# Kernel tuning notes

Measured on AMD Instinct MI355X. Metric: run time of the kernel, lower is better.

## Reference

```python
import jax, jax.numpy as jnp
import numpy as np

R = 16
LORA_ALPHA = 16
SCALING = LORA_ALPHA / R  # 1.0


def setup_inputs() -> dict:
    key = jax.random.key(0)
    kx, kr, ka = jax.random.split(key, 3)
    B, S, D, DO, E = 4, 2048, 4096, 4096, 8
    x = jax.random.normal(kx, (B, S, D), dtype=jnp.float32)
    # kaiming_uniform_(a=sqrt(5)) on Linear weight of fan_in=D -> U(-1/sqrt(D), 1/sqrt(D))
    bound_r = 1.0 / np.sqrt(D)
    route_w = jax.random.uniform(kr, (E, D), jnp.float32, -bound_r, bound_r)  # lora_route.weight
    bound_a = 1.0 / np.sqrt(D)
    A = jax.random.uniform(ka, (E, R, D), jnp.float32, -bound_a, bound_a)  # stacked lora_A{i}.weight [r, D]
    # lora_B weights are zero-initialized in the module; use small random for a nontrivial baseline
    kb = jax.random.fold_in(key, 7)
    Bw = jax.random.normal(kb, (E, DO, R), dtype=jnp.float32) * 0.02  # stacked lora_B{i}.weight [DO, r]
    return {"x": x, "route_w": route_w, "A": A, "Bw": Bw}


def reference(x, route_w, A, Bw):
    # router logits [B, S, E]
    logits = jnp.einsum("bsd,ed->bse", x, route_w)
    # top-1 hard routing: keep raw logit value at the argmax slot, zero elsewhere
    topk_v, topk_idx = jax.lax.top_k(logits, 1)  # [B,S,1]
    E = logits.shape[-1]
    route_weight = jax.nn.one_hot(topk_idx[..., 0], E, dtype=logits.dtype) * topk_v  # [B,S,E]
    # low-rank per-expert projections (dense over experts, as in the original loop)
    h = jnp.einsum("bsd,erd->bser", x, A)            # [B,S,E,r]
    wh = route_weight[..., None] * h                  # weight before the up-projection
    out = jnp.einsum("bser,eor->bso", wh, Bw) * SCALING  # [B,S,DO]
    return out
```

## Files before the change

### kernel.cpp

```cpp
#include <hip/hip_runtime.h>
#include <hip/hip_bf16.h>

#define DD   4096
#define NE   8
#define NR   16
#define NTOK 8192
#define NDO  4096
#define TAU  0.01f
#define MAXFLAG 8000

typedef __attribute__((ext_vector_type(8))) __bf16 bf16x8;
typedef __attribute__((ext_vector_type(4))) __bf16 bf16x4;
typedef __attribute__((ext_vector_type(4))) float  f32x4;

__device__ __forceinline__ bf16x8 to_bf16x8(float4 a, float4 b) {
    bf16x8 r;
    r[0] = (__bf16)a.x; r[1] = (__bf16)a.y; r[2] = (__bf16)a.z; r[3] = (__bf16)a.w;
    r[4] = (__bf16)b.x; r[5] = (__bf16)b.y; r[6] = (__bf16)b.z; r[7] = (__bf16)b.w;
    return r;
}

__device__ __forceinline__ bf16x8 zero_frag() {
    bf16x8 z;
    #pragma unroll
    for (int j = 0; j < 8; j++) z[j] = (__bf16)0.0f;
    return z;
}

__global__ __launch_bounds__(256) void k_prep_w(const float* __restrict__ rw,
                                                const float* __restrict__ Am,
                                                const float* __restrict__ Bw,
                                                __bf16* __restrict__ rwhl,
                                                __bf16* __restrict__ Ab,
                                                __bf16* __restrict__ Bwb) {
    const int b = blockIdx.x;
    if (b < 1024) {
        const int o = (b & 511) * 1024 + threadIdx.x * 4;
        const float4 v = *(const float4*)(((b < 512) ? Bw : Am) + o);
        bf16x4 p;
        p[0] = (__bf16)v.x; p[1] = (__bf16)v.y; p[2] = (__bf16)v.z; p[3] = (__bf16)v.w;
        *(bf16x4*)(((b < 512) ? Bwb : Ab) + o) = p;
    } else {
        const int o = (b - 1024) * 1024 + threadIdx.x * 4;
        const int row = o >> 12, k = o & 4095;
        const float4 v = *(const float4*)(rw + ((size_t)(row & 7) << 12) + k);
        bf16x4 p;
        if (row < 8) {
            p[0] = (__bf16)v.x; p[1] = (__bf16)v.y; p[2] = (__bf16)v.z; p[3] = (__bf16)v.w;
        } else {
            p[0] = (__bf16)(v.x - (float)(__bf16)v.x);
            p[1] = (__bf16)(v.y - (float)(__bf16)v.y);
            p[2] = (__bf16)(v.z - (float)(__bf16)v.z);
            p[3] = (__bf16)(v.w - (float)(__bf16)v.w);
        }
        *(bf16x4*)(rwhl + o) = p;
    }
}

__global__ __launch_bounds__(256, 1) void k_route(const float* __restrict__ x,
                                                  const __bf16* __restrict__ rwhl,
                                                  float* __restrict__ w_arr,
                                                  int*   __restrict__ token_list,
                                                  int*   __restrict__ count,
                                                  int*   __restrict__ nflag,
                                                  int*   __restrict__ flaglist) {
    const int t0   = blockIdx.x * 16;
    const int wv   = threadIdx.x >> 6;
    const int lane = threadIdx.x & 63;
    const int m    = lane & 15;
    const int half = lane >> 4;

    const float*  xrow = x    + (size_t)(t0 + m) * DD;
    const __bf16* wrow = rwhl + (size_t)m * DD;

    f32x4 acc = {0.f, 0.f, 0.f, 0.f};
    const int kbase = wv * 1024;
    for (int g = 0; g < 8; g++) {
        float4 xa[4], xc[4]; bf16x8 wb[4];
        #pragma unroll
        for (int i = 0; i < 4; i++) {
            const int k0 = kbase + (g * 4 + i) * 32 + half * 8;
            xa[i] = *(const float4*)(xrow + k0);
            xc[i] = *(const float4*)(xrow + k0 + 4);
            wb[i] = *(const bf16x8*)(wrow + k0);
        }
        #pragma unroll
        for (int i = 0; i < 4; i++)
            acc = __builtin_amdgcn_mfma_f32_16x16x32_bf16(to_bf16x8(xa[i], xc[i]), wb[i], acc, 0, 0, 0);
    }

    __shared__ float Lred[4][16][17];
    #pragma unroll
    for (int r = 0; r < 4; r++)
        Lred[wv][half * 4 + r][m] = acc[r];
    __syncthreads();

    __shared__ float logitS[16][NE];
    if (threadIdx.x < 128) {
        const int t = threadIdx.x >> 3, ee = threadIdx.x & 7;
        float s = 0.f;
        #pragma unroll
        for (int w = 0; w < 4; w++) s += Lred[w][t][ee] + Lred[w][t][ee + 8];
        logitS[t][ee] = s;
    }
    __syncthreads();

    if (threadIdx.x < 16) {
        const int t = threadIdx.x;
        float best = -1e30f, second = -1e30f; int be = 0;
        #pragma unroll
        for (int e = 0; e < NE; e++) {
            const float s = logitS[t][e];
            if (s > best) { second = best; best = s; be = e; }
            else if (s > second) { second = s; }
        }
        const int tok = t0 + t;
        w_arr[tok] = best;
        if (best - second < TAU) {
            const int p = atomicAdd(nflag, 1);
            if (p < MAXFLAG) flaglist[p] = tok;
        } else {
            const int p = atomicAdd(&count[be], 1);
            token_list[be * NTOK + p] = tok;
        }
    }
}

__global__ __launch_bounds__(256) void k_fix(const float* __restrict__ x,
                                             const float* __restrict__ rw,
                                             float* __restrict__ w_arr,
                                             int*   __restrict__ token_list,
                                             int*   __restrict__ count,
                                             const int* __restrict__ nflag,
                                             const int* __restrict__ flaglist) {
    const int wv   = threadIdx.x >> 6;
    const int lane = threadIdx.x & 63;
    int n = *nflag; if (n > MAXFLAG) n = MAXFLAG;

    for (int idx = blockIdx.x * 4 + wv; idx < n; idx += 512) {
        const int tok = flaglist[idx];
        const float* xp = x + (size_t)tok * DD;
        double acc[NE];
        #pragma unroll
        for (int e = 0; e < NE; e++) acc[e] = 0.0;
        for (int i = 0; i < 16; i++) {
            const int d4 = (i * 64 + lane) * 4;
            const float4 xv = *(const float4*)(xp + d4);
            const double x0 = xv.x, x1 = xv.y, x2 = xv.z, x3 = xv.w;
            #pragma unroll
            for (int e = 0; e < NE; e++) {
                const float4 wv4 = *(const float4*)(rw + (size_t)e * DD + d4);
                acc[e] = fma(x0, (double)wv4.x, acc[e]);
                acc[e] = fma(x1, (double)wv4.y, acc[e]);
                acc[e] = fma(x2, (double)wv4.z, acc[e]);
                acc[e] = fma(x3, (double)wv4.w, acc[e]);
            }
        }
        #pragma unroll
        for (int off = 32; off > 0; off >>= 1)
            #pragma unroll
            for (int e = 0; e < NE; e++)
                acc[e] += __shfl_xor(acc[e], off, 64);
        if (lane == 0) {
            double best = acc[0]; int be = 0;
            #pragma unroll
            for (int e = 1; e < NE; e++) if (acc[e] > best) { best = acc[e]; be = e; }
            w_arr[tok] = (float)best;
            const int pos = atomicAdd(&count[be], 1);
            token_list[be * NTOK + pos] = tok;
        }
    }
}

__global__ __launch_bounds__(1024) void k_h(const float* __restrict__ x,
                                            const __bf16* __restrict__ Ab,
                                            const float* __restrict__ w_arr,
                                            const int*   __restrict__ token_list,
                                            const int*   __restrict__ count,
                                            __hip_bfloat16* __restrict__ wh) {
    const int e    = blockIdx.x >> 7;
    const int g    = blockIdx.x & 127;
    const int cnt  = count[e];
    const int base = g * 32;
    if (base >= cnt) return;

    const int wv   = threadIdx.x >> 6;
    const int lane = threadIdx.x & 63;
    const int m    = lane & 15;
    const int half = lane >> 4;

    const int i0 = base + m,  i1 = base + 16 + m;
    const int tok0 = (i0 < cnt) ? token_list[e * NTOK + i0] : 0;
    const int tok1 = (i1 < cnt) ? token_list[e * NTOK + i1] : 0;
    const float*  xr0  = x  + (size_t)tok0 * DD;
    const float*  xr1  = x  + (size_t)tok1 * DD;
    const __bf16* arow = Ab + ((size_t)e * NR + m) * DD;

    f32x4 acc0 = {0.f,0.f,0.f,0.f}, acc1 = {0.f,0.f,0.f,0.f};
    const int kbase = wv * 256;
    #pragma unroll
    for (int kc = 0; kc < 8; kc++) {
        const int k0 = kbase + kc * 32 + half * 8;
        const bf16x8 bfrag = *(const bf16x8*)(arow + k0);
        const bf16x8 a0 = to_bf16x8(*(const float4*)(xr0 + k0),
                                    *(const float4*)(xr0 + k0 + 4));
        const bf16x8 a1 = to_bf16x8(*(const float4*)(xr1 + k0),
                                    *(const float4*)(xr1 + k0 + 4));
        acc0 = __builtin_amdgcn_mfma_f32_16x16x32_bf16(a0, bfrag, acc0, 0, 0, 0);
        acc1 = __builtin_amdgcn_mfma_f32_16x16x32_bf16(a1, bfrag, acc1, 0, 0, 0);
    }

    __shared__ float lds[16][32][17];
    #pragma unroll
    for (int rr = 0; rr < 4; rr++) {
        lds[wv][half * 4 + rr][m]      = acc0[rr];
        lds[wv][16 + half * 4 + rr][m] = acc1[rr];
    }
    __syncthreads();

    if (threadIdx.x < 512) {
        const int t = threadIdx.x >> 4;
        const int r = threadIdx.x & 15;
        const int i2 = base + t;
        if (i2 < cnt) {
            float s = 0.f;
            #pragma unroll
            for (int w = 0; w < 16; w++) s += lds[w][t][r];
            const int tk = token_list[e * NTOK + i2];
            wh[(size_t)tk * NR + r] = (__hip_bfloat16)(s * w_arr[tk]);
        }
    }
}

__global__ __launch_bounds__(256, 1) void k_out(const __bf16* __restrict__ Bwb,
                                                const __hip_bfloat16* __restrict__ wh,
                                                const int*   __restrict__ token_list,
                                                const int*   __restrict__ count,
                                                float* __restrict__ out) {
    const int bx    = blockIdx.x;
    const int chunk = bx & 3;
    const int slot  = (bx >> 2) & 511;
    const int e     = bx >> 11;
    const int cnt   = count[e];
    const int base  = slot * 16;
    if (base >= cnt) return;

    const int wv   = threadIdx.x >> 6;
    const int lane = threadIdx.x & 63;
    const int m    = lane & 15;
    const int half = lane >> 4;

    const int  idx   = base + m;
    const bool valid = idx < cnt;
    const int  tok   = valid ? token_list[e * NTOK + idx] : 0;
    const bf16x8 zf  = zero_frag();

    const bf16x8 a2 = (half < 2 && valid)
        ? *(const bf16x8*)((const __bf16*)wh + (size_t)tok * NR + half * 8)
        : zf;

    int trow[4]; bool vrow[4];
    #pragma unroll
    for (int r = 0; r < 4; r++) {
        const int ir = base + half * 4 + r;
        vrow[r] = ir < cnt;
        trow[r] = vrow[r] ? token_list[e * NTOK + ir] : 0;
    }

    const __bf16* bwe = Bwb + (size_t)e * NDO * NR;
    const int h2 = (half < 2) ? half : 0;
    const f32x4 zero4 = {0.f, 0.f, 0.f, 0.f};
    const int ob0 = chunk * 1024 + wv * 256;

    for (int g = 0; g < 2; g++) {
        bf16x8 B[8];
        #pragma unroll
        for (int i = 0; i < 8; i++) {
            const int obase = ob0 + (g * 8 + i) * 16;
            B[i] = (half < 2)
                ? *(const bf16x8*)(bwe + (size_t)(obase + m) * NR + h2 * 8)
                : zf;
        }
        #pragma unroll
        for (int i = 0; i < 8; i++) {
            const int obase = ob0 + (g * 8 + i) * 16;
            const f32x4 d = __builtin_amdgcn_mfma_f32_16x16x32_bf16(a2, B[i], zero4, 0, 0, 0);
            #pragma unroll
            for (int r = 0; r < 4; r++) {
                if (vrow[r])
                    __builtin_nontemporal_store(d[r], &out[(size_t)trow[r] * NDO + obase + m]);
            }
        }
    }
}

extern "C" void kernel_launch(void* const* d_in, const int* in_sizes, int n_in,
                              void* d_out, int out_size, void* d_ws, size_t ws_size,
                              hipStream_t stream) {
    const float* x  = (const float*)d_in[0];
    const float* rw = (const float*)d_in[1];
    const float* Am = (const float*)d_in[2];
    const float* Bw = (const float*)d_in[3];
    float* out = (float*)d_out;

    char* ws = (char*)d_ws;
    int*   count      = (int*)ws;
    int*   nflag      = (int*)(ws + 32);
    float* w_arr      = (float*)(ws + 512);
    int*   flaglist   = (int*)(ws + 33280);
    int*   token_list = (int*)(ws + 65536);
    __hip_bfloat16* wh = (__hip_bfloat16*)(ws + 327680);
    __bf16* rwhl      = (__bf16*)(ws + 589824);
    __bf16* Bwb       = (__bf16*)(ws + 720896);
    __bf16* Ab        = (__bf16*)(ws + 1769472);

    hipMemsetAsync(ws, 0, 64, stream);
    hipLaunchKernelGGL(k_prep_w, dim3(1088),  dim3(256),  0, stream, rw, Am, Bw, rwhl, Ab, Bwb);
    hipLaunchKernelGGL(k_route,  dim3(512),   dim3(256),  0, stream, x, rwhl, w_arr, token_list, count, nflag, flaglist);
    hipLaunchKernelGGL(k_fix,    dim3(128),   dim3(256),  0, stream, x, rw, w_arr, token_list, count, nflag, flaglist);
    hipLaunchKernelGGL(k_h,      dim3(1024),  dim3(1024), 0, stream, x, Ab, w_arr, token_list, count, wh);
    hipLaunchKernelGGL(k_out,    dim3(16384), dim3(256),  0, stream, Bwb, wh, token_list, count, out);
}
```

Baseline: 161.1 us.

## Split router GEMV over K across blocks and stage k_out stores through LDS

The router logit computation is split into four K-slices per token group, giving 2048 blocks instead of 512. Partial logits go to a workspace buffer, and a small finalize kernel sums them and does the top-1 selection and token bucketing. Separately, k_out now writes its MFMA results into a shared-memory tile and then emits full contiguous 1024-wide rows per token, replacing scattered per-lane stores. This adds a kernel launch, a partial-sum round trip through global memory, and about 64KB of LDS per k_out block, which may limit occupancy.

```diff
diff --git a/kernel.cpp b/kernel.cpp
--- a/kernel.cpp
+++ b/kernel.cpp
@@ -57,36 +57,29 @@
     }
 }
 
-__global__ __launch_bounds__(256, 1) void k_route(const float* __restrict__ x,
-                                                  const __bf16* __restrict__ rwhl,
-                                                  float* __restrict__ w_arr,
-                                                  int*   __restrict__ token_list,
-                                                  int*   __restrict__ count,
-                                                  int*   __restrict__ nflag,
-                                                  int*   __restrict__ flaglist) {
-    const int t0   = blockIdx.x * 16;
-    const int wv   = threadIdx.x >> 6;
+__global__ __launch_bounds__(256, 1) void k_route_part(const float* __restrict__ x,
+                                                       const __bf16* __restrict__ rwhl,
+                                                       float* __restrict__ pbuf) {
+    const int tg = blockIdx.x >> 2;
+    const int kg = blockIdx.x & 3;
+    const int t0 = tg * 16;
+    const int wv = threadIdx.x >> 6;
     const int lane = threadIdx.x & 63;
-    const int m    = lane & 15;
+    const int m = lane & 15;
     const int half = lane >> 4;
 
     const float*  xrow = x    + (size_t)(t0 + m) * DD;
     const __bf16* wrow = rwhl + (size_t)m * DD;
 
     f32x4 acc = {0.f, 0.f, 0.f, 0.f};
-    const int kbase = wv * 1024;
-    for (int g = 0; g < 8; g++) {
-        float4 xa[4], xc[4]; bf16x8 wb[4];
-        #pragma unroll
-        for (int i = 0; i < 4; i++) {
-            const int k0 = kbase + (g * 4 + i) * 32 + half * 8;
-            xa[i] = *(const float4*)(xrow + k0);
-            xc[i] = *(const float4*)(xrow + k0 + 4);
-            wb[i] = *(const bf16x8*)(wrow + k0);
-        }
-        #pragma unroll
-        for (int i = 0; i < 4; i++)
-            acc = __builtin_amdgcn_mfma_f32_16x16x32_bf16(to_bf16x8(xa[i], xc[i]), wb[i], acc, 0, 0, 0);
+    const int kbase = kg * 1024 + wv * 256;
+    #pragma unroll
+    for (int ks = 0; ks < 8; ks++) {
+        const int k0 = kbase + ks * 32 + half * 8;
+        const float4 xa = *(const float4*)(xrow + k0);
+        const float4 xc = *(const float4*)(xrow + k0 + 4);
+        const bf16x8 wb = *(const bf16x8*)(wrow + k0);
+        acc = __builtin_amdgcn_mfma_f32_16x16x32_bf16(to_bf16x8(xa, xc), wb, acc, 0, 0, 0);
     }
 
     __shared__ float Lred[4][16][17];
@@ -95,34 +88,43 @@
         Lred[wv][half * 4 + r][m] = acc[r];
     __syncthreads();
 
-    __shared__ float logitS[16][NE];
     if (threadIdx.x < 128) {
         const int t = threadIdx.x >> 3, ee = threadIdx.x & 7;
         float s = 0.f;
         #pragma unroll
         for (int w = 0; w < 4; w++) s += Lred[w][t][ee] + Lred[w][t][ee + 8];
-        logitS[t][ee] = s;
-    }
-    __syncthreads();
-
-    if (threadIdx.x < 16) {
-        const int t = threadIdx.x;
-        float best = -1e30f, second = -1e30f; int be = 0;
-        #pragma unroll
-        for (int e = 0; e < NE; e++) {
-            const float s = logitS[t][e];
-            if (s > best) { second = best; best = s; be = e; }
-            else if (s > second) { second = s; }
-        }
-        const int tok = t0 + t;
-        w_arr[tok] = best;
-        if (best - second < TAU) {
-            const int p = atomicAdd(nflag, 1);
-            if (p < MAXFLAG) flaglist[p] = tok;
-        } else {
-            const int p = atomicAdd(&count[be], 1);
-            token_list[be * NTOK + p] = tok;
-        }
+        pbuf[((size_t)kg * NTOK + t0 + t) * NE + ee] = s;
+    }
+}
+
+__global__ __launch_bounds__(256) void k_route_fin(const float* __restrict__ pbuf,
+                                                   float* __restrict__ w_arr,
+                                                   int*   __restrict__ token_list,
+                                                   int*   __restrict__ count,
+                                                   int*   __restrict__ nflag,
+                                                   int*   __restrict__ flaglist) {
+    const int tok = blockIdx.x * 256 + threadIdx.x;
+    float l[NE];
+    #pragma unroll
+    for (int e = 0; e < NE; e++)
+        l[e] = pbuf[((size_t)0 * NTOK + tok) * NE + e]
+             + pbuf[((size_t)1 * NTOK + tok) * NE + e]
+             + pbuf[((size_t)2 * NTOK + tok) * NE + e]
+             + pbuf[((size_t)3 * NTOK + tok) * NE + e];
+
+    float best = -1e30f, second = -1e30f; int be = 0;
+    #pragma unroll
+    for (int e = 0; e < NE; e++) {
+        if (l[e] > best) { second = best; best = l[e]; be = e; }
+        else if (l[e] > second) { second = l[e]; }
+    }
+    w_arr[tok] = best;
+    if (best - second < TAU) {
+        const int p = atomicAdd(nflag, 1);
+        if (p < MAXFLAG) flaglist[p] = tok;
+    } else {
+        const int p = atomicAdd(&count[be], 1);
+        token_list[be * NTOK + p] = tok;
     }
 }
 
@@ -259,37 +261,43 @@
         ? *(const bf16x8*)((const __bf16*)wh + (size_t)tok * NR + half * 8)
         : zf;
 
-    int trow[4]; bool vrow[4];
-    #pragma unroll
-    for (int r = 0; r < 4; r++) {
-        const int ir = base + half * 4 + r;
-        vrow[r] = ir < cnt;
-        trow[r] = vrow[r] ? token_list[e * NTOK + ir] : 0;
-    }
-
+    __shared__ float lds[16][1028];
     const __bf16* bwe = Bwb + (size_t)e * NDO * NR;
     const int h2 = (half < 2) ? half : 0;
     const f32x4 zero4 = {0.f, 0.f, 0.f, 0.f};
-    const int ob0 = chunk * 1024 + wv * 256;
+    const int ob0 = wv * 256;
 
     for (int g = 0; g < 2; g++) {
         bf16x8 B[8];
         #pragma unroll
         for (int i = 0; i < 8; i++) {
-            const int obase = ob0 + (g * 8 + i) * 16;
+            const int oc = chunk * 1024 + ob0 + (g * 8 + i) * 16;
             B[i] = (half < 2)
-                ? *(const bf16x8*)(bwe + (size_t)(obase + m) * NR + h2 * 8)
+                ? *(const bf16x8*)(bwe + (size_t)(oc + m) * NR + h2 * 8)
                 : zf;
         }
         #pragma unroll
         for (int i = 0; i < 8; i++) {
-            const int obase = ob0 + (g * 8 + i) * 16;
             const f32x4 d = __builtin_amdgcn_mfma_f32_16x16x32_bf16(a2, B[i], zero4, 0, 0, 0);
-            #pragma unroll
-            for (int r = 0; r < 4; r++) {
-                if (vrow[r])
-                    __builtin_nontemporal_store(d[r], &out[(size_t)trow[r] * NDO + obase + m]);
-            }
+            const int col = ob0 + (g * 8 + i) * 16 + m;
+            #pragma unroll
+            for (int r = 0; r < 4; r++)
+                lds[half * 4 + r][col] = d[r];
+        }
+    }
+    __syncthreads();
+
+    #pragma unroll 4
+    for (int r = 0; r < 16; r++) {
+        const int ir = base + r;
+        if (ir < cnt) {
+            const int tr = token_list[e * NTOK + ir];
+            const float4 v = *(const float4*)&lds[r][threadIdx.x * 4];
+            float* dst = out + (size_t)tr * NDO + chunk * 1024 + threadIdx.x * 4;
+            __builtin_nontemporal_store(v.x, dst + 0);
+            __builtin_nontemporal_store(v.y, dst + 1);
+            __builtin_nontemporal_store(v.z, dst + 2);
+            __builtin_nontemporal_store(v.w, dst + 3);
         }
     }
 }
@@ -313,11 +321,13 @@
     __bf16* rwhl      = (__bf16*)(ws + 589824);
     __bf16* Bwb       = (__bf16*)(ws + 720896);
     __bf16* Ab        = (__bf16*)(ws + 1769472);
+    float*  pbuf      = (float*)(ws + 3145728);
 
     hipMemsetAsync(ws, 0, 64, stream);
-    hipLaunchKernelGGL(k_prep_w, dim3(1088),  dim3(256),  0, stream, rw, Am, Bw, rwhl, Ab, Bwb);
-    hipLaunchKernelGGL(k_route,  dim3(512),   dim3(256),  0, stream, x, rwhl, w_arr, token_list, count, nflag, flaglist);
-    hipLaunchKernelGGL(k_fix,    dim3(128),   dim3(256),  0, stream, x, rw, w_arr, token_list, count, nflag, flaglist);
-    hipLaunchKernelGGL(k_h,      dim3(1024),  dim3(1024), 0, stream, x, Ab, w_arr, token_list, count, wh);
-    hipLaunchKernelGGL(k_out,    dim3(16384), dim3(256),  0, stream, Bwb, wh, token_list, count, out);
-}
+    hipLaunchKernelGGL(k_prep_w,     dim3(1088),  dim3(256), 0, stream, rw, Am, Bw, rwhl, Ab, Bwb);
+    hipLaunchKernelGGL(k_route_part, dim3(2048),  dim3(256), 0, stream, x, rwhl, pbuf);
+    hipLaunchKernelGGL(k_route_fin,  dim3(32),    dim3(256), 0, stream, pbuf, w_arr, token_list, count, nflag, flaglist);
+    hipLaunchKernelGGL(k_fix,        dim3(128),   dim3(256), 0, stream, x, rw, w_arr, token_list, count, nflag, flaglist);
+    hipLaunchKernelGGL(k_h,          dim3(1024),  dim3(1024),0, stream, x, Ab, w_arr, token_list, count, wh);
+    hipLaunchKernelGGL(k_out,        dim3(16384), dim3(256), 0, stream, Bwb, wh, token_list, count, out);
+}
```

Measured after the change: 149.2 us. -7.4%, faster.
